# Kernel tuning notes

Hardware: AMD Instinct MI355X
Metric: run time of the kernel (lower is better)

## Reference

```python
import jax, jax.numpy as jnp
import numpy as np


def setup_inputs() -> dict:
    key = jax.random.key(0)
    k1, k2, k3 = jax.random.split(key, 3)
    B, D = 4096, 512
    out_ftir = jax.random.normal(k1, (B, D), dtype=jnp.float32)
    out_raman = jax.random.normal(k2, (B, D), dtype=jnp.float32)
    labels = jax.random.randint(k3, (B,), 0, 1000, dtype=jnp.int64)
    # learned parameter: log_tau = log(1/init_tau), init_tau = 0.07
    log_tau = jnp.asarray(np.log(1.0 / 0.07), dtype=jnp.float32)
    return {"out_ftir": out_ftir, "out_raman": out_raman, "labels": labels, "log_tau": log_tau}


def reference(out_ftir, out_raman, labels, log_tau):
    # temperature scale, clamped above at 100
    tau = jnp.minimum(jnp.exp(log_tau), 100.0)
    # [B, B] similarity logits
    logits = (out_ftir @ out_raman.T) * tau
    # CLIP-style symmetric cross-entropy with diagonal targets (arange(B)).
    # Note: original torch code's loop over positive off-diagonal pairs
    # computes an unused tensor and does not affect the output.
    raman_lp = jnp.diagonal(jax.nn.log_softmax(logits, axis=-1))   # rows: ftir -> raman
    ftir_lp = jnp.diagonal(jax.nn.log_softmax(logits.T, axis=-1))  # cols: raman -> ftir
    raman_loss = -jnp.mean(raman_lp)
    ftir_loss = -jnp.mean(ftir_lp)
    return (ftir_loss + raman_loss) / 2.0
```

## Files before the change

### kernel.cpp

```cpp
#include <hip/hip_runtime.h>
#include <hip/hip_bf16.h>
#include <stdint.h>


typedef float f32x4 __attribute__((ext_vector_type(4)));
typedef __bf16 bf16x8 __attribute__((ext_vector_type(8)));
typedef __bf16 bf16x4 __attribute__((ext_vector_type(4)));

#define B_DIM 4096
#define D_DIM 512
#define NCHUNK 32

__device__ __forceinline__ void gld_lds16(const void* g, void* l) {
  __builtin_amdgcn_global_load_lds(
      (const __attribute__((address_space(1))) unsigned int*)g,
      (__attribute__((address_space(3))) unsigned int*)l,
      16, 0, 0);
}

__global__ __launch_bounds__(256) void cast_diag_kernel(
    const float* __restrict__ A, const float* __restrict__ Bm,
    __bf16* __restrict__ Abf, __bf16* __restrict__ Bbf,
    float* __restrict__ diagp, float* __restrict__ acc,
    unsigned* __restrict__ counter) {
  if (blockIdx.x == 0 && threadIdx.x == 0) { acc[0] = 0.f; counter[0] = 0u; }
  const float4* A4 = (const float4*)A;
  const float4* B4 = (const float4*)Bm;
  bf16x4* Ab4 = (bf16x4*)Abf;
  bf16x4* Bb4 = (bf16x4*)Bbf;
  int idx = blockIdx.x * 256 + threadIdx.x;
  float local = 0.f;
  #pragma unroll
  for (int it = 0; it < 4; ++it, idx += 512 * 256) {
    int row = idx >> 7, el4 = idx & 127;
    int g = (el4 >> 1) & 3;
    int gswz = g ^ ((row >> 1) & 3);
    int el4p = (el4 & ~6) | (gswz << 1);
    int pidx = row * 128 + el4p;
    float4 va = A4[idx], vb = B4[idx];
    bf16x4 oa, ob;
    oa[0] = (__bf16)va.x; oa[1] = (__bf16)va.y; oa[2] = (__bf16)va.z; oa[3] = (__bf16)va.w;
    ob[0] = (__bf16)vb.x; ob[1] = (__bf16)vb.y; ob[2] = (__bf16)vb.z; ob[3] = (__bf16)vb.w;
    Ab4[pidx] = oa; Bb4[pidx] = ob;
    local += va.x*vb.x + va.y*vb.y + va.z*vb.z + va.w*vb.w;
  }
  #pragma unroll
  for (int off = 1; off < 64; off <<= 1) local += __shfl_xor(local, off);
  __shared__ float red[4];
  int w = threadIdx.x >> 6, lane = threadIdx.x & 63;
  if (lane == 0) red[w] = local;
  __syncthreads();
  if (threadIdx.x == 0)
    diagp[blockIdx.x] = red[0] + red[1] + red[2] + red[3];
}

__global__ __launch_bounds__(256, 4) void gemm_lse_kernel(
    const __bf16* __restrict__ A, const __bf16* __restrict__ Bm,
    const float* __restrict__ log_tau,
    float* __restrict__ row_pmax, float* __restrict__ row_psum,
    float* __restrict__ col_pmax, float* __restrict__ col_psum) {
  __shared__ char smem[34816];
  const int blk = blockIdx.x;
  const int xcd = blk & 7, loc = blk >> 3;
  const int bm = (xcd & 3) * 8 + (loc & 7);
  const int bn = (xcd >> 2) * 16 + (loc >> 3);
  const int t = threadIdx.x;
  const int lane = t & 63;
  const int w = t >> 6;
  const int wm = (w >> 1) * 64, wn = (w & 1) * 64;
  const int q = lane >> 4, c16 = lane & 15;
  const int kbs = q ^ ((c16 >> 1) & 3);

  f32x4 acc[4][4] = {};

  const char* Ag = (const char*)A + (size_t)(bm * 128 + (t >> 2)) * 1024 + (t & 3) * 16;
  const char* Bg = (const char*)Bm + (size_t)(bn * 128 + (t >> 2)) * 1024 + (t & 3) * 16;

  #define ISSUE_STAGE(kt, p)                                                  \
    do {                                                                      \
      const char* ag = Ag + (kt) * 64;                                        \
      const char* bg = Bg + (kt) * 64;                                        \
      char* Al = smem + (p) * 16384 + t * 16;                                 \
      char* Bl = smem + (p) * 16384 + 8192 + t * 16;                          \
      _Pragma("unroll")                                                       \
      for (int i = 0; i < 2; ++i) {                                           \
        gld_lds16(ag + i * 65536, Al + i * 4096);                             \
        gld_lds16(bg + i * 65536, Bl + i * 4096);                             \
      }                                                                       \
    } while (0)

  ISSUE_STAGE(0, 0);
  for (int kt = 0; kt < 16; ++kt) {
    __syncthreads();
    if (kt < 15) ISSUE_STAGE(kt + 1, (kt + 1) & 1);
    const char* Ab = smem + (kt & 1) * 16384;
    const char* Bb = Ab + 8192;
    bf16x8 af[4], bfr[4];
    #pragma unroll
    for (int mi = 0; mi < 4; ++mi)
      af[mi] = *(const bf16x8*)(Ab + (wm + mi * 16 + c16) * 64 + kbs * 16);
    #pragma unroll
    for (int ni = 0; ni < 4; ++ni)
      bfr[ni] = *(const bf16x8*)(Bb + (wn + ni * 16 + c16) * 64 + kbs * 16);
    #pragma unroll
    for (int mi = 0; mi < 4; ++mi)
      #pragma unroll
      for (int ni = 0; ni < 4; ++ni)
        acc[mi][ni] = __builtin_amdgcn_mfma_f32_16x16x32_bf16(af[mi], bfr[ni], acc[mi][ni], 0, 0, 0);
  }
  __syncthreads();
  #undef ISSUE_STAGE

  const float tau = fminf(__expf(log_tau[0]), 100.0f);
  #pragma unroll
  for (int mi = 0; mi < 4; ++mi)
    #pragma unroll
    for (int ni = 0; ni < 4; ++ni)
      acc[mi][ni] *= tau;

  float2* rbuf = (float2*)smem;
  #pragma unroll
  for (int mi = 0; mi < 4; ++mi)
    #pragma unroll
    for (int r = 0; r < 4; ++r) {
      float v0 = acc[mi][0][r], v1 = acc[mi][1][r], v2 = acc[mi][2][r], v3 = acc[mi][3][r];
      float m = fmaxf(fmaxf(v0, v1), fmaxf(v2, v3));
      float s = __expf(v0 - m) + __expf(v1 - m) + __expf(v2 - m) + __expf(v3 - m);
      int R = wm + mi * 16 + q * 4 + r;
      rbuf[R * 33 + (w & 1) * 16 + c16] = make_float2(m, s);
    }
  __syncthreads();
  if (t < 128) {
    float M = rbuf[t * 33].x;
    #pragma unroll
    for (int x = 1; x < 32; ++x) M = fmaxf(M, rbuf[t * 33 + x].x);
    float S = 0.f;
    #pragma unroll
    for (int x = 0; x < 32; ++x) { float2 p = rbuf[t * 33 + x]; S += p.y * __expf(p.x - M); }
    row_pmax[bn * B_DIM + bm * 128 + t] = M;
    row_psum[bn * B_DIM + bm * 128 + t] = S;
  }
  __syncthreads();
  float2* cbuf = (float2*)smem;
  #pragma unroll
  for (int ni = 0; ni < 4; ++ni) {
    float m = -3.0e38f;
    #pragma unroll
    for (int mi = 0; mi < 4; ++mi)
      #pragma unroll
      for (int r = 0; r < 4; ++r) m = fmaxf(m, acc[mi][ni][r]);
    float s = 0.f;
    #pragma unroll
    for (int mi = 0; mi < 4; ++mi)
      #pragma unroll
      for (int r = 0; r < 4; ++r) s += __expf(acc[mi][ni][r] - m);
    int C = wn + ni * 16 + c16;
    cbuf[C * 9 + (w >> 1) * 4 + q] = make_float2(m, s);
  }
  __syncthreads();
  if (t < 128) {
    float M = cbuf[t * 9].x;
    #pragma unroll
    for (int y = 1; y < 8; ++y) M = fmaxf(M, cbuf[t * 9 + y].x);
    float S = 0.f;
    #pragma unroll
    for (int y = 0; y < 8; ++y) { float2 p = cbuf[t * 9 + y]; S += p.y * __expf(p.x - M); }
    col_pmax[bm * B_DIM + bn * 128 + t] = M;
    col_psum[bm * B_DIM + bn * 128 + t] = S;
  }
}

__global__ __launch_bounds__(256) void combine_kernel(
    const float* __restrict__ row_pmax, const float* __restrict__ row_psum,
    const float* __restrict__ col_pmax, const float* __restrict__ col_psum,
    const float* __restrict__ diagp, const float* __restrict__ log_tau,
    float* __restrict__ acc, unsigned* __restrict__ counter,
    float* __restrict__ out) {
  const int t = threadIdx.x;
  const int item = blockIdx.x * 256 + t;
  const float* pm; const float* ps; int i;
  if (item < B_DIM) { pm = row_pmax; ps = row_psum; i = item; }
  else              { pm = col_pmax; ps = col_psum; i = item - B_DIM; }
  float M = pm[i];
  #pragma unroll
  for (int k = 1; k < NCHUNK; ++k) M = fmaxf(M, pm[k * B_DIM + i]);
  float S = 0.f;
  #pragma unroll
  for (int k = 0; k < NCHUNK; ++k) S += ps[k * B_DIM + i] * __expf(pm[k * B_DIM + i] - M);
  float local = M + __logf(S);
  if (blockIdx.x == 0) {
    float tau = fminf(__expf(log_tau[0]), 100.0f);
    local += -2.0f * tau * (diagp[t] + diagp[t + 256]);
  }
  #pragma unroll
  for (int off = 1; off < 64; off <<= 1) local += __shfl_xor(local, off);
  __shared__ float red[4];
  int w = t >> 6, lane = t & 63;
  if (lane == 0) red[w] = local;
  __syncthreads();
  if (t == 0) {
    atomicAdd(acc, red[0] + red[1] + red[2] + red[3]);
    __threadfence();
    unsigned old = atomicAdd(counter, 1u);
    if (old == 31u) {
      float v = atomicAdd(acc, 0.0f);
      out[0] = v * (1.0f / 8192.0f);
    }
  }
}

extern "C" void kernel_launch(void* const* d_in, const int* in_sizes, int n_in,
                              void* d_out, int out_size, void* d_ws, size_t ws_size,
                              hipStream_t stream) {
  const float* ftir    = (const float*)d_in[0];
  const float* raman   = (const float*)d_in[1];
  const float* log_tau = (const float*)d_in[3];
  float* out = (float*)d_out;

  char* ws = (char*)d_ws;
  __bf16* Abf     = (__bf16*)(ws);
  __bf16* Bbf     = (__bf16*)(ws + (4u << 20));
  float* row_pmax = (float*)(ws + (8u << 20));
  float* row_psum = (float*)(ws + (8u << 20) + (512u << 10));
  float* col_pmax = (float*)(ws + (9u << 20));
  float* col_psum = (float*)(ws + (9u << 20) + (512u << 10));
  float* diagp    = (float*)(ws + (10u << 20));
  float* acc      = (float*)(ws + (10u << 20) + 4096);
  unsigned* cnt   = (unsigned*)(ws + (10u << 20) + 4096 + 4);

  cast_diag_kernel<<<512, 256, 0, stream>>>(ftir, raman, Abf, Bbf, diagp, acc, cnt);
  gemm_lse_kernel<<<1024, 256, 0, stream>>>(Abf, Bbf, log_tau,
                                            row_pmax, row_psum, col_pmax, col_psum);
  combine_kernel<<<32, 256, 0, stream>>>(row_pmax, row_psum, col_pmax, col_psum,
                                         diagp, log_tau, acc, cnt, out);
}
```

Before: 97.92 us.

## Enlarge GEMM tile to 256x128 per block with two-pass row LSE reduction

Doubles the M dimension of each GEMM block tile from 128 to 256 rows, so each wave holds an 8x4 MFMA accumulator grid and A/B fragments are reused across more MFMAs. The grid halves to 512 blocks, LDS grows to 48KB, and launch bounds drop to 2 blocks per CU. The row LSE epilogue is split into two 64-row passes to fit the shared buffer. The column partials drop to 16 chunks, and the combine kernel uses separate row and column chunk counts. The goal is less LDS and global traffic per FLOP, at the cost of higher register pressure, lower occupancy and fewer blocks than CUs for load balance.

```diff
diff --git a/kernel.cpp b/kernel.cpp
--- a/kernel.cpp
+++ b/kernel.cpp
@@ -9,7 +9,8 @@
 
 #define B_DIM 4096
 #define D_DIM 512
-#define NCHUNK 32
+#define NCHUNK_R 32
+#define NCHUNK_C 16
 
 __device__ __forceinline__ void gld_lds16(const void* g, void* l) {
   __builtin_amdgcn_global_load_lds(
@@ -54,56 +55,55 @@
     diagp[blockIdx.x] = red[0] + red[1] + red[2] + red[3];
 }
 
-__global__ __launch_bounds__(256, 4) void gemm_lse_kernel(
+__global__ __launch_bounds__(256, 2) void gemm_lse_kernel(
     const __bf16* __restrict__ A, const __bf16* __restrict__ Bm,
     const float* __restrict__ log_tau,
     float* __restrict__ row_pmax, float* __restrict__ row_psum,
     float* __restrict__ col_pmax, float* __restrict__ col_psum) {
-  __shared__ char smem[34816];
+  __shared__ char smem[49152];
   const int blk = blockIdx.x;
   const int xcd = blk & 7, loc = blk >> 3;
-  const int bm = (xcd & 3) * 8 + (loc & 7);
-  const int bn = (xcd >> 2) * 16 + (loc >> 3);
+  const int bm = (xcd & 3) * 4 + (loc & 3);
+  const int bn = (xcd >> 2) * 16 + (loc >> 2);
   const int t = threadIdx.x;
   const int lane = t & 63;
   const int w = t >> 6;
-  const int wm = (w >> 1) * 64, wn = (w & 1) * 64;
+  const int wm = (w >> 1) * 128, wn = (w & 1) * 64;
   const int q = lane >> 4, c16 = lane & 15;
   const int kbs = q ^ ((c16 >> 1) & 3);
 
-  f32x4 acc[4][4] = {};
-
-  const char* Ag = (const char*)A + (size_t)(bm * 128 + (t >> 2)) * 1024 + (t & 3) * 16;
+  f32x4 acc[8][4] = {};
+
+  const char* Ag = (const char*)A + (size_t)(bm * 256 + (t >> 2)) * 1024 + (t & 3) * 16;
   const char* Bg = (const char*)Bm + (size_t)(bn * 128 + (t >> 2)) * 1024 + (t & 3) * 16;
 
   #define ISSUE_STAGE(kt, p)                                                  \
     do {                                                                      \
       const char* ag = Ag + (kt) * 64;                                        \
       const char* bg = Bg + (kt) * 64;                                        \
-      char* Al = smem + (p) * 16384 + t * 16;                                 \
-      char* Bl = smem + (p) * 16384 + 8192 + t * 16;                          \
+      char* Al = smem + (p) * 24576 + t * 16;                                 \
+      char* Bl = smem + (p) * 24576 + 16384 + t * 16;                         \
       _Pragma("unroll")                                                       \
-      for (int i = 0; i < 2; ++i) {                                           \
-        gld_lds16(ag + i * 65536, Al + i * 4096);                             \
-        gld_lds16(bg + i * 65536, Bl + i * 4096);                             \
-      }                                                                       \
+      for (int i = 0; i < 4; ++i) gld_lds16(ag + i * 65536, Al + i * 4096);   \
+      _Pragma("unroll")                                                       \
+      for (int i = 0; i < 2; ++i) gld_lds16(bg + i * 65536, Bl + i * 4096);   \
     } while (0)
 
   ISSUE_STAGE(0, 0);
   for (int kt = 0; kt < 16; ++kt) {
     __syncthreads();
     if (kt < 15) ISSUE_STAGE(kt + 1, (kt + 1) & 1);
-    const char* Ab = smem + (kt & 1) * 16384;
-    const char* Bb = Ab + 8192;
-    bf16x8 af[4], bfr[4];
-    #pragma unroll
-    for (int mi = 0; mi < 4; ++mi)
+    const char* Ab = smem + (kt & 1) * 24576;
+    const char* Bb = Ab + 16384;
+    bf16x8 af[8], bfr[4];
+    #pragma unroll
+    for (int mi = 0; mi < 8; ++mi)
       af[mi] = *(const bf16x8*)(Ab + (wm + mi * 16 + c16) * 64 + kbs * 16);
     #pragma unroll
     for (int ni = 0; ni < 4; ++ni)
       bfr[ni] = *(const bf16x8*)(Bb + (wn + ni * 16 + c16) * 64 + kbs * 16);
     #pragma unroll
-    for (int mi = 0; mi < 4; ++mi)
+    for (int mi = 0; mi < 8; ++mi)
       #pragma unroll
       for (int ni = 0; ni < 4; ++ni)
         acc[mi][ni] = __builtin_amdgcn_mfma_f32_16x16x32_bf16(af[mi], bfr[ni], acc[mi][ni], 0, 0, 0);
@@ -113,49 +113,55 @@
 
   const float tau = fminf(__expf(log_tau[0]), 100.0f);
   #pragma unroll
-  for (int mi = 0; mi < 4; ++mi)
+  for (int mi = 0; mi < 8; ++mi)
     #pragma unroll
     for (int ni = 0; ni < 4; ++ni)
       acc[mi][ni] *= tau;
 
   float2* rbuf = (float2*)smem;
   #pragma unroll
-  for (int mi = 0; mi < 4; ++mi)
-    #pragma unroll
-    for (int r = 0; r < 4; ++r) {
-      float v0 = acc[mi][0][r], v1 = acc[mi][1][r], v2 = acc[mi][2][r], v3 = acc[mi][3][r];
-      float m = fmaxf(fmaxf(v0, v1), fmaxf(v2, v3));
-      float s = __expf(v0 - m) + __expf(v1 - m) + __expf(v2 - m) + __expf(v3 - m);
-      int R = wm + mi * 16 + q * 4 + r;
-      rbuf[R * 33 + (w & 1) * 16 + c16] = make_float2(m, s);
+  for (int p = 0; p < 2; ++p) {
+    #pragma unroll
+    for (int m4 = 0; m4 < 4; ++m4) {
+      int mi = p * 4 + m4;
+      #pragma unroll
+      for (int r = 0; r < 4; ++r) {
+        float v0 = acc[mi][0][r], v1 = acc[mi][1][r], v2 = acc[mi][2][r], v3 = acc[mi][3][r];
+        float m = fmaxf(fmaxf(v0, v1), fmaxf(v2, v3));
+        float s = __expf(v0 - m) + __expf(v1 - m) + __expf(v2 - m) + __expf(v3 - m);
+        int lrow = (w >> 1) * 64 + m4 * 16 + q * 4 + r;
+        rbuf[lrow * 33 + (w & 1) * 16 + c16] = make_float2(m, s);
+      }
     }
-  __syncthreads();
-  if (t < 128) {
-    float M = rbuf[t * 33].x;
-    #pragma unroll
-    for (int x = 1; x < 32; ++x) M = fmaxf(M, rbuf[t * 33 + x].x);
-    float S = 0.f;
-    #pragma unroll
-    for (int x = 0; x < 32; ++x) { float2 p = rbuf[t * 33 + x]; S += p.y * __expf(p.x - M); }
-    row_pmax[bn * B_DIM + bm * 128 + t] = M;
-    row_psum[bn * B_DIM + bm * 128 + t] = S;
-  }
-  __syncthreads();
+    __syncthreads();
+    if (t < 128) {
+      float M = rbuf[t * 33].x;
+      #pragma unroll
+      for (int x = 1; x < 32; ++x) M = fmaxf(M, rbuf[t * 33 + x].x);
+      float S = 0.f;
+      #pragma unroll
+      for (int x = 0; x < 32; ++x) { float2 pp = rbuf[t * 33 + x]; S += pp.y * __expf(pp.x - M); }
+      int grow = bm * 256 + (t >> 6) * 128 + p * 64 + (t & 63);
+      row_pmax[bn * B_DIM + grow] = M;
+      row_psum[bn * B_DIM + grow] = S;
+    }
+    __syncthreads();
+  }
   float2* cbuf = (float2*)smem;
   #pragma unroll
   for (int ni = 0; ni < 4; ++ni) {
     float m = -3.0e38f;
     #pragma unroll
-    for (int mi = 0; mi < 4; ++mi)
+    for (int mi = 0; mi < 8; ++mi)
       #pragma unroll
       for (int r = 0; r < 4; ++r) m = fmaxf(m, acc[mi][ni][r]);
     float s = 0.f;
     #pragma unroll
-    for (int mi = 0; mi < 4; ++mi)
+    for (int mi = 0; mi < 8; ++mi)
       #pragma unroll
       for (int r = 0; r < 4; ++r) s += __expf(acc[mi][ni][r] - m);
-    int C = wn + ni * 16 + c16;
-    cbuf[C * 9 + (w >> 1) * 4 + q] = make_float2(m, s);
+    int c = wn + ni * 16 + c16;
+    cbuf[c * 9 + (w >> 1) * 4 + q] = make_float2(m, s);
   }
   __syncthreads();
   if (t < 128) {
@@ -164,7 +170,7 @@
     for (int y = 1; y < 8; ++y) M = fmaxf(M, cbuf[t * 9 + y].x);
     float S = 0.f;
     #pragma unroll
-    for (int y = 0; y < 8; ++y) { float2 p = cbuf[t * 9 + y]; S += p.y * __expf(p.x - M); }
+    for (int y = 0; y < 8; ++y) { float2 pp = cbuf[t * 9 + y]; S += pp.y * __expf(pp.x - M); }
     col_pmax[bm * B_DIM + bn * 128 + t] = M;
     col_psum[bm * B_DIM + bn * 128 + t] = S;
   }
@@ -178,16 +184,28 @@
     float* __restrict__ out) {
   const int t = threadIdx.x;
   const int item = blockIdx.x * 256 + t;
-  const float* pm; const float* ps; int i;
-  if (item < B_DIM) { pm = row_pmax; ps = row_psum; i = item; }
-  else              { pm = col_pmax; ps = col_psum; i = item - B_DIM; }
-  float M = pm[i];
-  #pragma unroll
-  for (int k = 1; k < NCHUNK; ++k) M = fmaxf(M, pm[k * B_DIM + i]);
-  float S = 0.f;
-  #pragma unroll
-  for (int k = 0; k < NCHUNK; ++k) S += ps[k * B_DIM + i] * __expf(pm[k * B_DIM + i] - M);
-  float local = M + __logf(S);
+  float local;
+  if (item < B_DIM) {
+    const int i = item;
+    float M = row_pmax[i];
+    #pragma unroll
+    for (int k = 1; k < NCHUNK_R; ++k) M = fmaxf(M, row_pmax[k * B_DIM + i]);
+    float S = 0.f;
+    #pragma unroll
+    for (int k = 0; k < NCHUNK_R; ++k)
+      S += row_psum[k * B_DIM + i] * __expf(row_pmax[k * B_DIM + i] - M);
+    local = M + __logf(S);
+  } else {
+    const int i = item - B_DIM;
+    float M = col_pmax[i];
+    #pragma unroll
+    for (int k = 1; k < NCHUNK_C; ++k) M = fmaxf(M, col_pmax[k * B_DIM + i]);
+    float S = 0.f;
+    #pragma unroll
+    for (int k = 0; k < NCHUNK_C; ++k)
+      S += col_psum[k * B_DIM + i] * __expf(col_pmax[k * B_DIM + i] - M);
+    local = M + __logf(S);
+  }
   if (blockIdx.x == 0) {
     float tau = fminf(__expf(log_tau[0]), 100.0f);
     local += -2.0f * tau * (diagp[t] + diagp[t + 256]);
@@ -229,8 +247,8 @@
   unsigned* cnt   = (unsigned*)(ws + (10u << 20) + 4096 + 4);
 
   cast_diag_kernel<<<512, 256, 0, stream>>>(ftir, raman, Abf, Bbf, diagp, acc, cnt);
-  gemm_lse_kernel<<<1024, 256, 0, stream>>>(Abf, Bbf, log_tau,
-                                            row_pmax, row_psum, col_pmax, col_psum);
+  gemm_lse_kernel<<<512, 256, 0, stream>>>(Abf, Bbf, log_tau,
+                                           row_pmax, row_psum, col_pmax, col_psum);
   combine_kernel<<<32, 256, 0, stream>>>(row_pmax, row_psum, col_pmax, col_psum,
                                          diagp, log_tau, acc, cnt, out);
 }
```

New measurement: 99.38 us. Within noise of the previous version (+1.5%).

## Triple-buffer GEMM K-loop with explicit vmcnt waits instead of full syncs

Applied to the files above, without the earlier changes.

The bf16 GEMM main loop moves from double to triple buffering in LDS, issuing two stages ahead. It replaces __syncthreads with an explicit `s_waitcnt vmcnt(4)` plus a raw barrier, so the loads for the next stage stay in flight while the current stage computes. The aim is to hide global-to-LDS latency that the old full-drain sync exposed. The cost is more LDS per block (48KB), so occupancy drops from 4 to 3 blocks per CU. For the 1024-block grid this may add a partial second wave.

```diff
diff --git a/kernel.cpp b/kernel.cpp
--- a/kernel.cpp
+++ b/kernel.cpp
@@ -54,12 +54,12 @@
     diagp[blockIdx.x] = red[0] + red[1] + red[2] + red[3];
 }
 
-__global__ __launch_bounds__(256, 4) void gemm_lse_kernel(
+__global__ __launch_bounds__(256, 3) void gemm_lse_kernel(
     const __bf16* __restrict__ A, const __bf16* __restrict__ Bm,
     const float* __restrict__ log_tau,
     float* __restrict__ row_pmax, float* __restrict__ row_psum,
     float* __restrict__ col_pmax, float* __restrict__ col_psum) {
-  __shared__ char smem[34816];
+  __shared__ char smem[49152];
   const int blk = blockIdx.x;
   const int xcd = blk & 7, loc = blk >> 3;
   const int bm = (xcd & 3) * 8 + (loc & 7);
@@ -89,27 +89,41 @@
       }                                                                       \
     } while (0)
 
+  #define COMPUTE(p)                                                          \
+    do {                                                                      \
+      const char* Ab = smem + (p) * 16384;                                    \
+      const char* Bb = Ab + 8192;                                             \
+      bf16x8 af[4], bfr[4];                                                   \
+      _Pragma("unroll")                                                       \
+      for (int mi = 0; mi < 4; ++mi)                                          \
+        af[mi] = *(const bf16x8*)(Ab + (wm + mi * 16 + c16) * 64 + kbs * 16); \
+      _Pragma("unroll")                                                       \
+      for (int ni = 0; ni < 4; ++ni)                                          \
+        bfr[ni] = *(const bf16x8*)(Bb + (wn + ni * 16 + c16) * 64 + kbs * 16);\
+      _Pragma("unroll")                                                       \
+      for (int mi = 0; mi < 4; ++mi)                                          \
+        _Pragma("unroll")                                                     \
+        for (int ni = 0; ni < 4; ++ni)                                        \
+          acc[mi][ni] = __builtin_amdgcn_mfma_f32_16x16x32_bf16(              \
+              af[mi], bfr[ni], acc[mi][ni], 0, 0, 0);                         \
+    } while (0)
+
   ISSUE_STAGE(0, 0);
-  for (int kt = 0; kt < 16; ++kt) {
-    __syncthreads();
-    if (kt < 15) ISSUE_STAGE(kt + 1, (kt + 1) & 1);
-    const char* Ab = smem + (kt & 1) * 16384;
-    const char* Bb = Ab + 8192;
-    bf16x8 af[4], bfr[4];
-    #pragma unroll
-    for (int mi = 0; mi < 4; ++mi)
-      af[mi] = *(const bf16x8*)(Ab + (wm + mi * 16 + c16) * 64 + kbs * 16);
-    #pragma unroll
-    for (int ni = 0; ni < 4; ++ni)
-      bfr[ni] = *(const bf16x8*)(Bb + (wn + ni * 16 + c16) * 64 + kbs * 16);
-    #pragma unroll
-    for (int mi = 0; mi < 4; ++mi)
-      #pragma unroll
-      for (int ni = 0; ni < 4; ++ni)
-        acc[mi][ni] = __builtin_amdgcn_mfma_f32_16x16x32_bf16(af[mi], bfr[ni], acc[mi][ni], 0, 0, 0);
-  }
+  ISSUE_STAGE(1, 1);
+  for (int kt = 0; kt < 15; ++kt) {
+    asm volatile("s_waitcnt vmcnt(4)" ::: "memory");
+    __builtin_amdgcn_s_barrier();
+    asm volatile("" ::: "memory");
+    if (kt < 14) ISSUE_STAGE(kt + 2, (kt + 2) % 3);
+    COMPUTE(kt % 3);
+  }
+  asm volatile("s_waitcnt vmcnt(0)" ::: "memory");
+  __builtin_amdgcn_s_barrier();
+  asm volatile("" ::: "memory");
+  COMPUTE(15 % 3);
   __syncthreads();
   #undef ISSUE_STAGE
+  #undef COMPUTE
 
   const float tau = fminf(__expf(log_tau[0]), 100.0f);
   #pragma unroll
```

After: 96.82 us. No clear change (-1.1%).
